# Performance work log

Measured on AMD Instinct MI355X. Metric: run time of the kernel, lower is better.

## Reference

```python
import jax, jax.numpy as jnp
import numpy as np

NUM_HEADS = 16
HEAD_DIM = 64
HIDDEN = 1024
ROPE_BASE = 10000.0


def _rope_cache(seq_len, dtype):
    inv_freq = 1.0 / (ROPE_BASE ** (jnp.arange(0, HEAD_DIM, 2, dtype=jnp.float32) / HEAD_DIM))
    freqs = jnp.arange(seq_len, dtype=jnp.float32)[:, None] * inv_freq[None, :]  # [S, D/2]
    emb = jnp.concatenate([freqs, freqs], axis=-1)  # [S, D]
    return jnp.cos(emb).astype(dtype), jnp.sin(emb).astype(dtype)


def _rotate_half(x):
    x1, x2 = jnp.split(x, 2, axis=-1)
    return jnp.concatenate([-x2, x1], axis=-1)


def setup_inputs() -> dict:
    key = jax.random.key(0)
    k1, k2, k3 = jax.random.split(key, 3)
    B, S = 1, 4096
    x = jax.random.normal(k1, (B, S, HIDDEN), dtype=jnp.float32)
    w_qkv = jax.random.normal(k2, (3 * HIDDEN, HIDDEN), dtype=jnp.float32) * (1.0 / np.sqrt(HIDDEN))
    w_out = jax.random.normal(k3, (HIDDEN, HIDDEN), dtype=jnp.float32) * (1.0 / np.sqrt(HIDDEN))
    return {"x": x, "w_qkv": w_qkv, "w_out": w_out}


def reference(x, w_qkv, w_out):
    B, S, _ = x.shape
    scale = 1.0 / np.sqrt(HEAD_DIM)
    # fused QKV projection (torch Linear: x @ W^T)
    qkv = jnp.einsum('bsd,ed->bse', x, w_qkv)
    qkv = qkv.reshape(B, S, 3, NUM_HEADS, HEAD_DIM).transpose(2, 0, 3, 1, 4)
    q, k, v = qkv[0], qkv[1], qkv[2]  # [B, H, S, Dh]
    cos, sin = _rope_cache(S, x.dtype)  # [S, Dh]
    cos = cos[None, None]
    sin = sin[None, None]
    q = q * cos + _rotate_half(q) * sin
    k = k * cos + _rotate_half(k) * sin
    scores = jnp.einsum('bhqd,bhkd->bhqk', q, k) * scale  # [B, H, S, S]
    causal = jnp.triu(jnp.ones((S, S), dtype=bool), k=1)
    min_val = jnp.finfo(scores.dtype).min
    scores = jnp.where(causal[None, None], min_val, scores)
    attn = jax.nn.softmax(scores, axis=-1)
    out = jnp.einsum('bhqk,bhkd->bhqd', attn, v)  # [B, H, S, Dh]
    out = out.transpose(0, 2, 1, 3).reshape(B, S, HIDDEN)
    return jnp.einsum('bsd,ed->bse', out, w_out)
```

## Files before the change

kernel.cpp:

```cpp
#include <hip/hip_runtime.h>

#define S_LEN 4096
#define NHEAD 16
#define DHEAD 64
#define HID 1024

typedef float f32x4 __attribute__((ext_vector_type(4)));
typedef float f32x16 __attribute__((ext_vector_type(16)));
typedef unsigned short u16x8 __attribute__((ext_vector_type(8)));
typedef __bf16 bf16x8 __attribute__((ext_vector_type(8)));

__device__ __forceinline__ unsigned short f2bf(float f) {
  union { float f; unsigned u; } x; x.f = f;
  return (unsigned short)((x.u + 0x7FFFu + ((x.u >> 16) & 1u)) >> 16);
}
__device__ __forceinline__ float bf2f(unsigned short u) {
  union { unsigned u; float f; } x; x.u = ((unsigned)u) << 16;
  return x.f;
}
__device__ __forceinline__ f32x4 mfma16(u16x8 a, u16x8 b, f32x4 c) {
  return __builtin_amdgcn_mfma_f32_16x16x32_bf16(
      __builtin_bit_cast(bf16x8, a), __builtin_bit_cast(bf16x8, b), c, 0, 0, 0);
}
__device__ __forceinline__ f32x16 mfma32(u16x8 a, u16x8 b, f32x16 c) {
  return __builtin_amdgcn_mfma_f32_32x32x16_bf16(
      __builtin_bit_cast(bf16x8, a), __builtin_bit_cast(bf16x8, b), c, 0, 0, 0);
}
__device__ __forceinline__ void gload16(const void* g, void* l) {
  __builtin_amdgcn_global_load_lds(
      (const __attribute__((address_space(1))) void*)g,
      (__attribute__((address_space(3))) void*)l, 16, 0, 0);
}
__device__ __forceinline__ void permswap(unsigned& a, unsigned& b) {
#if __has_builtin(__builtin_amdgcn_permlane32_swap)
  typedef unsigned u32x2 __attribute__((ext_vector_type(2)));
  u32x2 r = __builtin_amdgcn_permlane32_swap(a, b, false, false);
  a = r[0]; b = r[1];
#else
  asm volatile("v_permlane32_swap_b32 %0, %1" : "+v"(a), "+v"(b));
#endif
}
__device__ __forceinline__ unsigned cvtpk(float lo, float hi) {
  unsigned r;
  asm("v_cvt_pk_bf16_f32 %0, %1, %2" : "=v"(r) : "v"(lo), "v"(hi));
  return r;
}
__device__ __forceinline__ float fexp2(float x) {
  float r;
  asm("v_exp_f32 %0, %1" : "=v"(r) : "v"(x));
  return r;
}

__global__ void k_cvt_all(const float4* __restrict__ x, const float4* __restrict__ wq,
                          const float4* __restrict__ wo, ushort4* __restrict__ xb,
                          ushort4* __restrict__ wqb, ushort4* __restrict__ wob) {
  int i = blockIdx.x * blockDim.x + threadIdx.x;
  const float4* src; ushort4* dst; int off;
  if (i < 1048576)      { src = x;  dst = xb;  off = i; }
  else if (i < 1835008) { src = wq; dst = wqb; off = i - 1048576; }
  else                  { src = wo; dst = wob; off = i - 1835008; }
  float4 v = src[off];
  ushort4 o;
  o.x = f2bf(v.x); o.y = f2bf(v.y); o.z = f2bf(v.z); o.w = f2bf(v.w);
  dst[off] = o;
}

__global__ void k_rope_split(const unsigned short* __restrict__ qkv,
                             unsigned short* __restrict__ Q,
                             unsigned short* __restrict__ Kf) {
  int s = blockIdx.x;
  int t = threadIdx.x;
  int h = t >> 5, i = t & 31;
  float inv = fexp2(-(float)i * 0.4152410118609203f);
  float ang = (float)s * inv;
  float sn, cs;
  __sincosf(ang, &sn, &cs);
  const unsigned short* row = qkv + (size_t)s * 3072;
  float q1 = bf2f(row[h * 64 + i]);
  float q2 = bf2f(row[h * 64 + i + 32]);
  float k1 = bf2f(row[1024 + h * 64 + i]);
  float k2 = bf2f(row[1024 + h * 64 + i + 32]);
  const float ksc = 0.125f * 1.44269504f;
  size_t qo = ((size_t)h * S_LEN + s) * 64 + i;
  Q[qo]      = f2bf(q1 * cs - q2 * sn);
  Q[qo + 32] = f2bf(q2 * cs + q1 * sn);
  int t32 = s >> 5, kv = s & 31;
  size_t ko = ((((size_t)h * 128 + t32) * 4 + (i >> 4)) * 2 + ((i >> 3) & 1)) * 256 + kv * 8 + (i & 7);
  Kf[ko]        = f2bf((k1 * cs - k2 * sn) * ksc);
  Kf[ko + 1024] = f2bf((k2 * cs + k1 * sn) * ksc);
}

__global__ void k_vt(const unsigned short* __restrict__ qkv,
                     unsigned short* __restrict__ Vf) {
  __shared__ unsigned short tile[64][65];
  int st = blockIdx.x, h = blockIdx.y;
  int t = threadIdx.x;
  int r = t >> 2, c0 = (t & 3) * 16;
  const unsigned short* src = qkv + (size_t)(st * 64 + r) * 3072 + 2048 + h * 64 + c0;
  u16x8 a = *(const u16x8*)src;
  u16x8 b = *(const u16x8*)(src + 8);
#pragma unroll
  for (int j = 0; j < 8; ++j) { tile[r][c0 + j] = a[j]; tile[r][c0 + 8 + j] = b[j]; }
  __syncthreads();
#pragma unroll
  for (int pass = 0; pass < 2; ++pass) {
    int task = t + pass * 256;
    int o = task >> 6, d = task & 63;
    int t32 = st * 2 + (o >> 2), kc = (o >> 1) & 1, hfv = o & 1;
    u16x8 v;
#pragma unroll
    for (int e = 0; e < 8; ++e) v[e] = tile[o * 8 + e][d];
    *(u16x8*)(Vf + (((((size_t)h * 128 + t32) * 2 + kc) * 2 + hfv) * 64 + d) * 8) = v;
  }
}

__device__ __forceinline__ void stc(float* p, float v) { *p = v; }
__device__ __forceinline__ void stc(unsigned short* p, float v) { *p = f2bf(v); }

template <typename OutT>
__global__ __launch_bounds__(256, 3) void gemm_bt(
    const unsigned short* __restrict__ A, const unsigned short* __restrict__ B,
    OutT* __restrict__ C, int M, int N, int K) {
  __shared__ __attribute__((aligned(16))) unsigned short As[3][128][32];
  __shared__ __attribute__((aligned(16))) unsigned short Bs[3][128][32];
  const int tid = threadIdx.x;
  const int w = tid >> 6, lane = tid & 63;
  const int bm = blockIdx.y * 128, bn = blockIdx.x * 128;
  const int wr = w >> 1, wc = w & 1;
  const int l16 = lane >> 2;
  const int c4s = ((lane & 3) ^ ((lane >> 3) & 3)) * 8;
  f32x4 acc[4][4] = {};

  auto stage = [&](int buf, int kt) {
    const int k0 = kt << 5;
#pragma unroll
    for (int c = 0; c < 2; ++c) {
      int row = w * 32 + c * 16;
      gload16(A + (size_t)(bm + row + l16) * K + k0 + c4s, &As[buf][row][0]);
      gload16(B + (size_t)(bn + row + l16) * K + k0 + c4s, &Bs[buf][row][0]);
    }
  };

  const int nk = K >> 5;
  stage(0, 0);
  stage(1, 1);
  int cur = 0;
  for (int kt = 0; kt < nk; ++kt) {
    asm volatile("s_waitcnt vmcnt(4)" ::: "memory");
    __builtin_amdgcn_sched_barrier(0);
    __builtin_amdgcn_s_barrier();
    __builtin_amdgcn_sched_barrier(0);
    {
      const int sbuf = (cur + 2 >= 3) ? cur - 1 : cur + 2;
      const int stile = (kt + 2 < nk) ? kt + 2 : nk - 1;
      stage(sbuf, stile);
    }
    const int sph = (((lane >> 4) ^ (lane >> 1)) & 3) * 16;
    u16x8 af[4], bfr[4];
#pragma unroll
    for (int m = 0; m < 4; ++m) {
      int row = wr * 64 + m * 16 + (lane & 15);
      af[m] = *(const u16x8*)((const char*)&As[cur][0][0] + row * 64 + sph);
    }
#pragma unroll
    for (int n = 0; n < 4; ++n) {
      int row = wc * 64 + n * 16 + (lane & 15);
      bfr[n] = *(const u16x8*)((const char*)&Bs[cur][0][0] + row * 64 + sph);
    }
#pragma unroll
    for (int m = 0; m < 4; ++m)
#pragma unroll
      for (int n = 0; n < 4; ++n)
        acc[m][n] = mfma16(af[m], bfr[n], acc[m][n]);
    cur = (cur + 1 == 3) ? 0 : cur + 1;
  }
#pragma unroll
  for (int m = 0; m < 4; ++m) {
    int row = bm + wr * 64 + m * 16 + (lane >> 4) * 4;
#pragma unroll
    for (int n = 0; n < 4; ++n) {
      int col = bn + wc * 64 + n * 16 + (lane & 15);
#pragma unroll
      for (int j = 0; j < 4; ++j) stc(&C[(size_t)(row + j) * N + col], acc[m][n][j]);
    }
  }
}

__device__ __forceinline__ void attn_range(
    const unsigned short* __restrict__ kfb, const unsigned short* __restrict__ vfb,
    const u16x8* qf, f32x16& accA, f32x16& accB, float& l_own,
    int t0, int t1, int nst, int qg, int hf, int kOffBase, int vOffBase) {
  u16x8 ka[4], kb_[4], kc2[4], va[4], vb_[4], vc2[4];
#define LOADK(dst, t)                                                         \
  {                                                                           \
    const unsigned short* p_ = kfb + (size_t)(t) * 2048 + kOffBase;           \
    dst[0] = *(const u16x8*)(p_);                                             \
    dst[1] = *(const u16x8*)(p_ + 512);                                       \
    dst[2] = *(const u16x8*)(p_ + 1024);                                      \
    dst[3] = *(const u16x8*)(p_ + 1536);                                      \
  }
#define LOADV(dst, t)                                                         \
  {                                                                           \
    const unsigned short* p_ = vfb + (size_t)(t) * 2048 + vOffBase;           \
    dst[0] = *(const u16x8*)(p_);                                             \
    dst[1] = *(const u16x8*)(p_ + 256);                                       \
    dst[2] = *(const u16x8*)(p_ + 1024);                                      \
    dst[3] = *(const u16x8*)(p_ + 1280);                                      \
  }
#define STEP(t, kc_, vc_, kn_, vn_)                                           \
  {                                                                           \
    const int tn = ((t) + 2 < t1) ? (t) + 2 : t1 - 1;                         \
    LOADK(kn_, tn);                                                           \
    LOADV(vn_, tn);                                                           \
    f32x16 sc = {};                                                           \
    __builtin_amdgcn_s_setprio(1);                                            \
    _Pragma("unroll") for (int c = 0; c < 4; ++c) sc = mfma32(kc_[c], qf[c], sc); \
    __builtin_amdgcn_s_setprio(0);                                            \
    if ((t) == nst - 1) {                     \
      _Pragma("unroll") for (int r = 0; r < 16; ++r) {                        \
        int kvl = (t) * 32 + (r & 3) + 8 * (r >> 2) + 4 * hf;                 \
        if (kvl > qg) sc[r] = -1e30f;                                         \
      }                                                                       \
    }                                                                         \
    float p[16];                                                              \
    _Pragma("unroll") for (int r = 0; r < 16; ++r) p[r] = fexp2(sc[r]);       \
    l_own += (((p[0] + p[1]) + (p[2] + p[3])) + ((p[4] + p[5]) + (p[6] + p[7]))) + \
             (((p[8] + p[9]) + (p[10] + p[11])) + ((p[12] + p[13]) + (p[14] + p[15]))); \
    unsigned dw[8];                                                           \
    _Pragma("unroll") for (int k = 0; k < 8; ++k) dw[k] = cvtpk(p[2 * k], p[2 * k + 1]); \
    __builtin_amdgcn_s_setprio(1);                                            \
    _Pragma("unroll") for (int kc = 0; kc < 2; ++kc) {                        \
      unsigned x0 = dw[4 * kc + 0], x1 = dw[4 * kc + 1];                      \
      unsigned y0 = dw[4 * kc + 2], y1 = dw[4 * kc + 3];                      \
      permswap(x0, y0);                                                       \
      permswap(x1, y1);                                                       \
      union { u16x8 v; unsigned u[4]; } pf;                                   \
      pf.u[0] = x0; pf.u[1] = x1; pf.u[2] = y0; pf.u[3] = y1;                 \
      accA = mfma32(vc_[kc * 2 + 0], pf.v, accA);                             \
      accB = mfma32(vc_[kc * 2 + 1], pf.v, accB);                             \
    }                                                                         \
    __builtin_amdgcn_s_setprio(0);                                            \
  }

  LOADK(ka, t0);
  LOADV(va, t0);
  {
    const int t1c = (t0 + 1 < t1) ? t0 + 1 : t1 - 1;
    LOADK(kb_, t1c);
    LOADV(vb_, t1c);
  }
  int t = t0;
  while (true) {
    STEP(t, ka, va, kc2, vc2);
    if (++t >= t1) break;
    STEP(t, kb_, vb_, ka, va);
    if (++t >= t1) break;
    STEP(t, kc2, vc2, kb_, vb_);
    if (++t >= t1) break;
  }
#undef STEP
#undef LOADK
#undef LOADV
}

__device__ __forceinline__ void attn_epilogue(
    const f32x16& accA, const f32x16& accB, float l_own, char* eb,
    unsigned short* __restrict__ O, int h, int qb, int wr, int q31, int hf) {
  float l_run;
  {
    unsigned a = __float_as_uint(l_own), b = a;
    permswap(a, b);
    l_run = __uint_as_float(a) + __uint_as_float(b);
  }
  const float inv = 1.0f / l_run;
#pragma unroll
  for (int dblk = 0; dblk < 2; ++dblk) {
#pragma unroll
    for (int tt = 0; tt < 4; ++tt) {
      float a0, a1, a2, a3;
      if (dblk == 0) { a0 = accA[4 * tt]; a1 = accA[4 * tt + 1]; a2 = accA[4 * tt + 2]; a3 = accA[4 * tt + 3]; }
      else           { a0 = accB[4 * tt]; a1 = accB[4 * tt + 1]; a2 = accB[4 * tt + 2]; a3 = accB[4 * tt + 3]; }
      unsigned d0 = cvtpk(a0 * inv, a1 * inv);
      unsigned d1 = cvtpk(a2 * inv, a3 * inv);
      int dbase = dblk * 32 + 8 * tt + 4 * hf;
      int off = (q31 * 128 + dbase * 2) ^ ((q31 & 7) << 4);
      *(uint2*)(eb + off) = make_uint2(d0, d1);
    }
  }
  const int lane = hf * 32 + q31;
#pragma unroll
  for (int pass = 0; pass < 4; ++pass) {
    int q = (lane >> 3) + pass * 8;
    int c8 = lane & 7;
    u16x8 vv = *(const u16x8*)(eb + ((q * 128 + c8 * 16) ^ ((q & 7) << 4)));
    *(u16x8*)(O + (size_t)(qb + wr * 32 + q) * HID + h * 64 + c8 * 8) = vv;
  }
}

__global__ __launch_bounds__(512) void flash_attn(
    const unsigned short* __restrict__ Q,
    const unsigned short* __restrict__ Kf,
    const unsigned short* __restrict__ Vf,
    unsigned short* __restrict__ O) {
  __shared__ __attribute__((aligned(16))) unsigned short ebuf[8][2048];
  __shared__ float part[4][64][33];
  const int tid = threadIdx.x;
  const int wv = tid >> 6, lane = tid & 63;
  const int wr = wv & 3, role = wv >> 2;
  const int q31 = lane & 31, hf = lane >> 5;
  const int h = blockIdx.x;
  const int p = blockIdx.y;
  const int tileB = 31 - p;
  const int nstA = 4 * p + wr + 1;
  const int nstB = 4 * tileB + wr + 1;
  const int cut = 62 - 4 * p;

  const unsigned short* kfb = Kf + (size_t)h * 128 * 2048;
  const unsigned short* vfb = Vf + (size_t)h * 128 * 2048;
  const int kOffBase = hf * 256 + q31 * 8;
  const int vOffBase = hf * 512 + q31 * 8;
  char* eb = (char*)&ebuf[wv][0];

  const int qgB = tileB * 128 + wr * 32 + q31;
  u16x8 qfB[4];
  {
    const unsigned short* qp = Q + ((size_t)h * S_LEN + qgB) * 64 + hf * 8;
#pragma unroll
    for (int c = 0; c < 4; ++c) qfB[c] = *(const u16x8*)(qp + c * 16);
  }

  if (role == 0) {
    const int qgA = p * 128 + wr * 32 + q31;
    u16x8 qfA[4];
    {
      const unsigned short* qp = Q + ((size_t)h * S_LEN + qgA) * 64 + hf * 8;
#pragma unroll
      for (int c = 0; c < 4; ++c) qfA[c] = *(const u16x8*)(qp + c * 16);
    }
    f32x16 accA = {}, accB = {};
    float l_own = 0.f;
    attn_range(kfb, vfb, qfA, accA, accB, l_own, 0, nstA, nstA, qgA, hf, kOffBase, vOffBase);
    attn_epilogue(accA, accB, l_own, eb, O, h, p * 128, wr, q31, hf);
    f32x16 bA = {}, bB = {};
    float bl = 0.f;
    attn_range(kfb, vfb, qfB, bA, bB, bl, 0, cut, nstB, qgB, hf, kOffBase, vOffBase);
    float* pp = &part[wr][lane][0];
#pragma unroll
    for (int r = 0; r < 16; ++r) { pp[r] = bA[r]; pp[16 + r] = bB[r]; }
    pp[32] = bl;
    __syncthreads();
  } else {
    f32x16 bA = {}, bB = {};
    float bl = 0.f;
    attn_range(kfb, vfb, qfB, bA, bB, bl, cut, nstB, nstB, qgB, hf, kOffBase, vOffBase);
    __syncthreads();
    const float* pp = &part[wr][lane][0];
#pragma unroll
    for (int r = 0; r < 16; ++r) { bA[r] += pp[r]; bB[r] += pp[16 + r]; }
    bl += pp[32];
    attn_epilogue(bA, bB, bl, eb, O, h, tileB * 128, wr, q31, hf);
  }
}

extern "C" void kernel_launch(void* const* d_in, const int* in_sizes, int n_in,
                              void* d_out, int out_size, void* d_ws, size_t ws_size,
                              hipStream_t stream) {
  const float* x = (const float*)d_in[0];
  const float* w_qkv = (const float*)d_in[1];
  const float* w_out = (const float*)d_in[2];
  float* out = (float*)d_out;
  char* ws = (char*)d_ws;

  unsigned short* xb    = (unsigned short*)(ws + 0);
  unsigned short* wqkvb = (unsigned short*)(ws + 8388608);
  unsigned short* woutb = (unsigned short*)(ws + 14680064);
  unsigned short* qkvb  = (unsigned short*)(ws + 16777216);
  unsigned short* Qb    = (unsigned short*)(ws + 41943040);
  unsigned short* Kfb   = (unsigned short*)(ws + 50331648);
  unsigned short* Vfb   = (unsigned short*)(ws + 58720256);
  unsigned short* attnb = (unsigned short*)(ws + 67108864);

  k_cvt_all<<<dim3(8192), dim3(256), 0, stream>>>(
      (const float4*)x, (const float4*)w_qkv, (const float4*)w_out,
      (ushort4*)xb, (ushort4*)wqkvb, (ushort4*)woutb);

  gemm_bt<unsigned short><<<dim3(24, 32), dim3(256), 0, stream>>>(xb, wqkvb, qkvb, 4096, 3072, 1024);

  k_rope_split<<<dim3(4096), dim3(512), 0, stream>>>(qkvb, Qb, Kfb);
  k_vt<<<dim3(64, 16), dim3(256), 0, stream>>>(qkvb, Vfb);

  flash_attn<<<dim3(16, 16), dim3(512), 0, stream>>>(Qb, Kfb, Vfb, attnb);

  gemm_bt<float><<<dim3(8, 32), dim3(256), 0, stream>>>(attnb, woutb, out, 4096, 1024, 1024);
}
```

Measured before the change: 130.1 us.

## Split attention KV range across four wave groups with strided tiles

The attention block grows from 512 to 1024 threads. Each of four wave roles now processes every fourth KV tile for both the A and B query tiles, and the partial accumulators are merged through shared memory. This replaces the earlier two-role split with a contiguous cut, with the aim of raising parallelism and balancing load across waves within a block. In exchange it adds an extra barrier, more shared-memory traffic for the partial sums, and higher register pressure under launch_bounds(1024).

```diff
diff --git a/kernel.cpp b/kernel.cpp
--- a/kernel.cpp
+++ b/kernel.cpp
@@ -186,10 +186,12 @@
   }
 }
 
-__device__ __forceinline__ void attn_range(
+__device__ __forceinline__ void attn_range4(
     const unsigned short* __restrict__ kfb, const unsigned short* __restrict__ vfb,
     const u16x8* qf, f32x16& accA, f32x16& accB, float& l_own,
-    int t0, int t1, int nst, int qg, int hf, int kOffBase, int vOffBase) {
+    int r, int nst, int qg, int hf, int kOffBase, int vOffBase) {
+  if (r >= nst) return;
+  const int last = r + ((nst - 1 - r) >> 2) * 4;
   u16x8 ka[4], kb_[4], kc2[4], va[4], vb_[4], vc2[4];
 #define LOADK(dst, t)                                                         \
   {                                                                           \
@@ -207,9 +209,9 @@
     dst[2] = *(const u16x8*)(p_ + 1024);                                      \
     dst[3] = *(const u16x8*)(p_ + 1280);                                      \
   }
-#define STEP(t, kc_, vc_, kn_, vn_)                                           \
+#define STEP(t, kc_, vc_, kn_, vn_)                                          \
   {                                                                           \
-    const int tn = ((t) + 2 < t1) ? (t) + 2 : t1 - 1;                         \
+    const int tn = ((t) + 8 <= last) ? (t) + 8 : last;                        \
     LOADK(kn_, tn);                                                           \
     LOADV(vn_, tn);                                                           \
     f32x16 sc = {};                                                           \
@@ -217,13 +219,13 @@
     _Pragma("unroll") for (int c = 0; c < 4; ++c) sc = mfma32(kc_[c], qf[c], sc); \
     __builtin_amdgcn_s_setprio(0);                                            \
     if ((t) == nst - 1) {                     \
-      _Pragma("unroll") for (int r = 0; r < 16; ++r) {                        \
-        int kvl = (t) * 32 + (r & 3) + 8 * (r >> 2) + 4 * hf;                 \
-        if (kvl > qg) sc[r] = -1e30f;                                         \
+      _Pragma("unroll") for (int rr = 0; rr < 16; ++rr) {                     \
+        int kvl = (t) * 32 + (rr & 3) + 8 * (rr >> 2) + 4 * hf;               \
+        if (kvl > qg) sc[rr] = -1e30f;                                        \
       }                                                                       \
     }                                                                         \
     float p[16];                                                              \
-    _Pragma("unroll") for (int r = 0; r < 16; ++r) p[r] = fexp2(sc[r]);       \
+    _Pragma("unroll") for (int rr = 0; rr < 16; ++rr) p[rr] = fexp2(sc[rr]);  \
     l_own += (((p[0] + p[1]) + (p[2] + p[3])) + ((p[4] + p[5]) + (p[6] + p[7]))) + \
              (((p[8] + p[9]) + (p[10] + p[11])) + ((p[12] + p[13]) + (p[14] + p[15]))); \
     unsigned dw[8];                                                           \
@@ -242,21 +244,21 @@
     __builtin_amdgcn_s_setprio(0);                                            \
   }
 
-  LOADK(ka, t0);
-  LOADV(va, t0);
+  LOADK(ka, r);
+  LOADV(va, r);
   {
-    const int t1c = (t0 + 1 < t1) ? t0 + 1 : t1 - 1;
+    const int t1c = (r + 4 <= last) ? r + 4 : last;
     LOADK(kb_, t1c);
     LOADV(vb_, t1c);
   }
-  int t = t0;
+  int t = r;
   while (true) {
     STEP(t, ka, va, kc2, vc2);
-    if (++t >= t1) break;
+    t += 4; if (t > last) break;
     STEP(t, kb_, vb_, ka, va);
-    if (++t >= t1) break;
+    t += 4; if (t > last) break;
     STEP(t, kc2, vc2, kb_, vb_);
-    if (++t >= t1) break;
+    t += 4; if (t > last) break;
   }
 #undef STEP
 #undef LOADK
@@ -297,13 +299,13 @@
   }
 }
 
-__global__ __launch_bounds__(512) void flash_attn(
+__global__ __launch_bounds__(1024, 4) void flash_attn(
     const unsigned short* __restrict__ Q,
     const unsigned short* __restrict__ Kf,
     const unsigned short* __restrict__ Vf,
     unsigned short* __restrict__ O) {
-  __shared__ __attribute__((aligned(16))) unsigned short ebuf[8][2048];
-  __shared__ float part[4][64][33];
+  __shared__ __attribute__((aligned(16))) unsigned short ebuf[4][2048];
+  __shared__ float part[3][4][64][34];
   const int tid = threadIdx.x;
   const int wv = tid >> 6, lane = tid & 63;
   const int wr = wv & 3, role = wv >> 2;
@@ -313,52 +315,68 @@
   const int tileB = 31 - p;
   const int nstA = 4 * p + wr + 1;
   const int nstB = 4 * tileB + wr + 1;
-  const int cut = 62 - 4 * p;
 
   const unsigned short* kfb = Kf + (size_t)h * 128 * 2048;
   const unsigned short* vfb = Vf + (size_t)h * 128 * 2048;
   const int kOffBase = hf * 256 + q31 * 8;
   const int vOffBase = hf * 512 + q31 * 8;
-  char* eb = (char*)&ebuf[wv][0];
-
-  const int qgB = tileB * 128 + wr * 32 + q31;
-  u16x8 qfB[4];
+  char* eb = (char*)&ebuf[wr][0];
+
   {
-    const unsigned short* qp = Q + ((size_t)h * S_LEN + qgB) * 64 + hf * 8;
-#pragma unroll
-    for (int c = 0; c < 4; ++c) qfB[c] = *(const u16x8*)(qp + c * 16);
-  }
-
-  if (role == 0) {
     const int qgA = p * 128 + wr * 32 + q31;
     u16x8 qfA[4];
-    {
-      const unsigned short* qp = Q + ((size_t)h * S_LEN + qgA) * 64 + hf * 8;
-#pragma unroll
-      for (int c = 0; c < 4; ++c) qfA[c] = *(const u16x8*)(qp + c * 16);
-    }
-    f32x16 accA = {}, accB = {};
-    float l_own = 0.f;
-    attn_range(kfb, vfb, qfA, accA, accB, l_own, 0, nstA, nstA, qgA, hf, kOffBase, vOffBase);
-    attn_epilogue(accA, accB, l_own, eb, O, h, p * 128, wr, q31, hf);
+    const unsigned short* qp = Q + ((size_t)h * S_LEN + qgA) * 64 + hf * 8;
+#pragma unroll
+    for (int c = 0; c < 4; ++c) qfA[c] = *(const u16x8*)(qp + c * 16);
+    f32x16 aA = {}, aB = {};
+    float al = 0.f;
+    attn_range4(kfb, vfb, qfA, aA, aB, al, role, nstA, qgA, hf, kOffBase, vOffBase);
+    if (role != 0) {
+      float* pp = &part[role - 1][wr][lane][0];
+#pragma unroll
+      for (int r = 0; r < 16; ++r) { pp[r] = aA[r]; pp[16 + r] = aB[r]; }
+      pp[32] = al;
+    }
+    __syncthreads();
+    if (role == 0) {
+#pragma unroll
+      for (int s = 0; s < 3; ++s) {
+        const float* pp = &part[s][wr][lane][0];
+#pragma unroll
+        for (int r = 0; r < 16; ++r) { aA[r] += pp[r]; aB[r] += pp[16 + r]; }
+        al += pp[32];
+      }
+    }
+    __syncthreads();
+    if (role == 0) attn_epilogue(aA, aB, al, eb, O, h, p * 128, wr, q31, hf);
+  }
+
+  {
+    const int qgB = tileB * 128 + wr * 32 + q31;
+    u16x8 qfB[4];
+    const unsigned short* qp = Q + ((size_t)h * S_LEN + qgB) * 64 + hf * 8;
+#pragma unroll
+    for (int c = 0; c < 4; ++c) qfB[c] = *(const u16x8*)(qp + c * 16);
     f32x16 bA = {}, bB = {};
     float bl = 0.f;
-    attn_range(kfb, vfb, qfB, bA, bB, bl, 0, cut, nstB, qgB, hf, kOffBase, vOffBase);
-    float* pp = &part[wr][lane][0];
-#pragma unroll
-    for (int r = 0; r < 16; ++r) { pp[r] = bA[r]; pp[16 + r] = bB[r]; }
-    pp[32] = bl;
+    attn_range4(kfb, vfb, qfB, bA, bB, bl, role, nstB, qgB, hf, kOffBase, vOffBase);
+    if (role != 3) {
+      float* pp = &part[role][wr][lane][0];
+#pragma unroll
+      for (int r = 0; r < 16; ++r) { pp[r] = bA[r]; pp[16 + r] = bB[r]; }
+      pp[32] = bl;
+    }
     __syncthreads();
-  } else {
-    f32x16 bA = {}, bB = {};
-    float bl = 0.f;
-    attn_range(kfb, vfb, qfB, bA, bB, bl, cut, nstB, nstB, qgB, hf, kOffBase, vOffBase);
-    __syncthreads();
-    const float* pp = &part[wr][lane][0];
-#pragma unroll
-    for (int r = 0; r < 16; ++r) { bA[r] += pp[r]; bB[r] += pp[16 + r]; }
-    bl += pp[32];
-    attn_epilogue(bA, bB, bl, eb, O, h, tileB * 128, wr, q31, hf);
+    if (role == 3) {
+#pragma unroll
+      for (int s = 0; s < 3; ++s) {
+        const float* pp = &part[s][wr][lane][0];
+#pragma unroll
+        for (int r = 0; r < 16; ++r) { bA[r] += pp[r]; bB[r] += pp[16 + r]; }
+        bl += pp[32];
+      }
+      attn_epilogue(bA, bB, bl, eb, O, h, tileB * 128, wr, q31, hf);
+    }
   }
 }
 
@@ -389,7 +407,7 @@
   k_rope_split<<<dim3(4096), dim3(512), 0, stream>>>(qkvb, Qb, Kfb);
   k_vt<<<dim3(64, 16), dim3(256), 0, stream>>>(qkvb, Vfb);
 
-  flash_attn<<<dim3(16, 16), dim3(512), 0, stream>>>(Qb, Kfb, Vfb, attnb);
+  flash_attn<<<dim3(16, 16), dim3(1024), 0, stream>>>(Qb, Kfb, Vfb, attnb);
 
   gemm_bt<float><<<dim3(8, 32), dim3(256), 0, stream>>>(attnb, woutb, out, 4096, 1024, 1024);
 }
```

New measurement: 448.6 us. +244.8%, slower.

## Split each query tile's KV range evenly across two wave groups, one tile per block

Applied to the files above, without the earlier changes.

Instead of pairing a short and a long causal query tile per block (role 0 doing a full short tile plus part of the long one), each block now handles a single query tile and both wave groups split its KV steps in half, merging partials via shared memory. The grid doubles to 512 blocks, with heavy tiles scheduled first. This is meant to balance work between the two wave groups and improve occupancy and load balance. The trade-off is more blocks that each repeat the Q loads and the partial-merge sync, and shorter per-block pipelines for small tiles.

```diff
diff --git a/kernel.cpp b/kernel.cpp
--- a/kernel.cpp
+++ b/kernel.cpp
@@ -190,6 +190,7 @@
     const unsigned short* __restrict__ kfb, const unsigned short* __restrict__ vfb,
     const u16x8* qf, f32x16& accA, f32x16& accB, float& l_own,
     int t0, int t1, int nst, int qg, int hf, int kOffBase, int vOffBase) {
+  if (t0 >= t1) return;
   u16x8 ka[4], kb_[4], kc2[4], va[4], vb_[4], vc2[4];
 #define LOADK(dst, t)                                                         \
   {                                                                           \
@@ -217,13 +218,13 @@
     _Pragma("unroll") for (int c = 0; c < 4; ++c) sc = mfma32(kc_[c], qf[c], sc); \
     __builtin_amdgcn_s_setprio(0);                                            \
     if ((t) == nst - 1) {                     \
-      _Pragma("unroll") for (int r = 0; r < 16; ++r) {                        \
-        int kvl = (t) * 32 + (r & 3) + 8 * (r >> 2) + 4 * hf;                 \
-        if (kvl > qg) sc[r] = -1e30f;                                         \
+      _Pragma("unroll") for (int rr = 0; rr < 16; ++rr) {                     \
+        int kvl = (t) * 32 + (rr & 3) + 8 * (rr >> 2) + 4 * hf;               \
+        if (kvl > qg) sc[rr] = -1e30f;                                        \
       }                                                                       \
     }                                                                         \
     float p[16];                                                              \
-    _Pragma("unroll") for (int r = 0; r < 16; ++r) p[r] = fexp2(sc[r]);       \
+    _Pragma("unroll") for (int rr = 0; rr < 16; ++rr) p[rr] = fexp2(sc[rr]);  \
     l_own += (((p[0] + p[1]) + (p[2] + p[3])) + ((p[4] + p[5]) + (p[6] + p[7]))) + \
              (((p[8] + p[9]) + (p[10] + p[11])) + ((p[12] + p[13]) + (p[14] + p[15]))); \
     unsigned dw[8];                                                           \
@@ -302,63 +303,48 @@
     const unsigned short* __restrict__ Kf,
     const unsigned short* __restrict__ Vf,
     unsigned short* __restrict__ O) {
-  __shared__ __attribute__((aligned(16))) unsigned short ebuf[8][2048];
-  __shared__ float part[4][64][33];
+  __shared__ __attribute__((aligned(16))) unsigned short ebuf[4][2048];
+  __shared__ float part[4][64][34];
   const int tid = threadIdx.x;
   const int wv = tid >> 6, lane = tid & 63;
   const int wr = wv & 3, role = wv >> 2;
   const int q31 = lane & 31, hf = lane >> 5;
   const int h = blockIdx.x;
-  const int p = blockIdx.y;
-  const int tileB = 31 - p;
-  const int nstA = 4 * p + wr + 1;
-  const int nstB = 4 * tileB + wr + 1;
-  const int cut = 62 - 4 * p;
+  const int y = blockIdx.y;
+  const int qt = (y < 16) ? (31 - y) : (y - 16);
+  const int nst = 4 * qt + wr + 1;
+  const int cut = (nst + 1) >> 1;
 
   const unsigned short* kfb = Kf + (size_t)h * 128 * 2048;
   const unsigned short* vfb = Vf + (size_t)h * 128 * 2048;
   const int kOffBase = hf * 256 + q31 * 8;
   const int vOffBase = hf * 512 + q31 * 8;
-  char* eb = (char*)&ebuf[wv][0];
-
-  const int qgB = tileB * 128 + wr * 32 + q31;
-  u16x8 qfB[4];
+
+  const int qg = qt * 128 + wr * 32 + q31;
+  u16x8 qf[4];
   {
-    const unsigned short* qp = Q + ((size_t)h * S_LEN + qgB) * 64 + hf * 8;
-#pragma unroll
-    for (int c = 0; c < 4; ++c) qfB[c] = *(const u16x8*)(qp + c * 16);
-  }
-
+    const unsigned short* qp = Q + ((size_t)h * S_LEN + qg) * 64 + hf * 8;
+#pragma unroll
+    for (int c = 0; c < 4; ++c) qf[c] = *(const u16x8*)(qp + c * 16);
+  }
+
+  f32x16 aA = {}, aB = {};
+  float al = 0.f;
   if (role == 0) {
-    const int qgA = p * 128 + wr * 32 + q31;
-    u16x8 qfA[4];
-    {
-      const unsigned short* qp = Q + ((size_t)h * S_LEN + qgA) * 64 + hf * 8;
-#pragma unroll
-      for (int c = 0; c < 4; ++c) qfA[c] = *(const u16x8*)(qp + c * 16);
-    }
-    f32x16 accA = {}, accB = {};
-    float l_own = 0.f;
-    attn_range(kfb, vfb, qfA, accA, accB, l_own, 0, nstA, nstA, qgA, hf, kOffBase, vOffBase);
-    attn_epilogue(accA, accB, l_own, eb, O, h, p * 128, wr, q31, hf);
-    f32x16 bA = {}, bB = {};
-    float bl = 0.f;
-    attn_range(kfb, vfb, qfB, bA, bB, bl, 0, cut, nstB, qgB, hf, kOffBase, vOffBase);
+    attn_range(kfb, vfb, qf, aA, aB, al, 0, cut, nst, qg, hf, kOffBase, vOffBase);
     float* pp = &part[wr][lane][0];
 #pragma unroll
-    for (int r = 0; r < 16; ++r) { pp[r] = bA[r]; pp[16 + r] = bB[r]; }
-    pp[32] = bl;
+    for (int r = 0; r < 16; ++r) { pp[r] = aA[r]; pp[16 + r] = aB[r]; }
+    pp[32] = al;
     __syncthreads();
   } else {
-    f32x16 bA = {}, bB = {};
-    float bl = 0.f;
-    attn_range(kfb, vfb, qfB, bA, bB, bl, cut, nstB, nstB, qgB, hf, kOffBase, vOffBase);
+    attn_range(kfb, vfb, qf, aA, aB, al, cut, nst, nst, qg, hf, kOffBase, vOffBase);
     __syncthreads();
     const float* pp = &part[wr][lane][0];
 #pragma unroll
-    for (int r = 0; r < 16; ++r) { bA[r] += pp[r]; bB[r] += pp[16 + r]; }
-    bl += pp[32];
-    attn_epilogue(bA, bB, bl, eb, O, h, tileB * 128, wr, q31, hf);
+    for (int r = 0; r < 16; ++r) { aA[r] += pp[r]; aB[r] += pp[16 + r]; }
+    al += pp[32];
+    attn_epilogue(aA, aB, al, (char*)&ebuf[wr][0], O, h, qt * 128, wr, q31, hf);
   }
 }
 
@@ -389,7 +375,7 @@
   k_rope_split<<<dim3(4096), dim3(512), 0, stream>>>(qkvb, Qb, Kfb);
   k_vt<<<dim3(64, 16), dim3(256), 0, stream>>>(qkvb, Vfb);
 
-  flash_attn<<<dim3(16, 16), dim3(512), 0, stream>>>(Qb, Kfb, Vfb, attnb);
+  flash_attn<<<dim3(16, 32), dim3(512), 0, stream>>>(Qb, Kfb, Vfb, attnb);
 
   gemm_bt<float><<<dim3(8, 32), dim3(256), 0, stream>>>(attnb, woutb, out, 4096, 1024, 1024);
 }
```

Result: slower. 140.4 us (+7.9%).
